# Kernel optimization log

Measured on AMD Instinct MI355X. Metric: run time of the kernel, lower is better.

The kernel has to match this reference:

```python
import jax, jax.numpy as jnp
import numpy as np

D, H, K = 384, 6, 8

def _ln(x, g, b, eps=1e-5):
    mu = jnp.mean(x, axis=-1, keepdims=True)
    var = jnp.mean((x - mu) ** 2, axis=-1, keepdims=True)
    return (x - mu) * jax.lax.rsqrt(var + eps) * g + b

def setup_inputs() -> dict:
    key = jax.random.key(0)
    ks = jax.random.split(key, 20)
    B, N = 4, 2048
    s = 0.02
    inp = {
        'x': jax.random.normal(ks[0], (B, N, D), jnp.float32),
        'knn_index': jax.random.randint(ks[1], (B * K * N,), 0, B * N, jnp.int64),
        'ln1_g': jnp.ones((D,), jnp.float32),
        'ln1_b': jnp.zeros((D,), jnp.float32),
        'w_qkv': jax.random.normal(ks[2], (D, 3 * D), jnp.float32) * s,
        'w_proj': jax.random.normal(ks[3], (D, D), jnp.float32) * s,
        'b_proj': jnp.zeros((D,), jnp.float32),
        'w_knn': jax.random.normal(ks[4], (2 * D, D), jnp.float32) * s,
        'b_knn': jnp.zeros((D,), jnp.float32),
        'w_g1': jax.random.normal(ks[5], (2 * D, D), jnp.float32) * s,
        'b_g1': jnp.zeros((D,), jnp.float32),
        'w_g2': jax.random.normal(ks[6], (D, D), jnp.float32) * s,
        'b_g2': jnp.zeros((D,), jnp.float32),
        'ln2_g': jnp.ones((D,), jnp.float32),
        'ln2_b': jnp.zeros((D,), jnp.float32),
        'w_fc1': jax.random.normal(ks[7], (D, 4 * D), jnp.float32) * s,
        'b_fc1': jnp.zeros((4 * D,), jnp.float32),
        'w_fc2': jax.random.normal(ks[8], (4 * D, D), jnp.float32) * s,
        'b_fc2': jnp.zeros((D,), jnp.float32),
    }
    return inp

def reference(x, knn_index, ln1_g, ln1_b, w_qkv, w_proj, b_proj, w_knn, b_knn,
              w_g1, b_g1, w_g2, b_g2, ln2_g, ln2_b, w_fc1, b_fc1, w_fc2, b_fc2):
    B, N, _ = x.shape
    hd = D // H
    scale = hd ** -0.5
    nx = _ln(x, ln1_g, ln1_b)
    # --- self attention ---
    qkv = (nx @ w_qkv).reshape(B, N, 3, H, hd).transpose(2, 0, 3, 1, 4)  # [3,B,H,N,hd]
    q, k, v = qkv[0], qkv[1], qkv[2]
    attn = jax.nn.softmax(jnp.einsum('bhnd,bhmd->bhnm', q * scale, k), axis=-1)
    attn_out = jnp.einsum('bhnm,bhmd->bhnd', attn, v).transpose(0, 2, 1, 3).reshape(B, N, D)
    attn_out = attn_out @ w_proj + b_proj
    # --- EdgeConv-style graph feature: gather-concat-MLP-maxpool ---
    feat = nx.reshape(B * N, D)[knn_index].reshape(B, K, N, D)
    xe = jnp.broadcast_to(nx[:, None], (B, K, N, D))
    gf = jnp.concatenate([feat - xe, xe], axis=-1)  # [B,K,N,2D]
    knn_out = jnp.max(jax.nn.leaky_relu(gf @ w_knn + b_knn, 0.2), axis=1)  # [B,N,D]
    # --- salience gate ---
    gi = jnp.concatenate([attn_out, knn_out], axis=-1)
    gate = jax.nn.sigmoid(jax.nn.gelu(gi @ w_g1 + b_g1, approximate=False) @ w_g2 + b_g2)
    fused = (1 - gate) * attn_out + gate * knn_out
    x = x + fused
    # --- FFN ---
    h = jax.nn.gelu(_ln(x, ln2_g, ln2_b) @ w_fc1 + b_fc1, approximate=False)
    x = x + (h @ w_fc2 + b_fc2)
    return x
```

## Files before the change

kernel.cpp:

```cpp
#include <hip/hip_runtime.h>
#include <math.h>

typedef unsigned short u16;
typedef __attribute__((ext_vector_type(8))) short short8;
typedef __attribute__((ext_vector_type(4))) float floatx4;
typedef __attribute__((ext_vector_type(4))) short sh4v;

union sh4u { sh4v v; u16 u[4]; };
union sh8u { short8 v; u16 u[8]; };

__device__ __forceinline__ floatx4 mfma16(short8 a, short8 b, floatx4 c) {
  return __builtin_amdgcn_mfma_f32_16x16x32_bf16(a, b, c, 0, 0, 0);
}

__device__ __forceinline__ floatx4 zero4() {
  floatx4 z = {0.f, 0.f, 0.f, 0.f};
  return z;
}

__device__ __forceinline__ u16 f2b(float f) {
  union { float f; unsigned u; } v; v.f = f;
  unsigned u = v.u;
  return (u16)((u + 0x7FFFu + ((u >> 16) & 1u)) >> 16);
}

__device__ __forceinline__ float b2f(u16 u) {
  union { unsigned u; float f; } v; v.u = ((unsigned)u) << 16;
  return v.f;
}

__device__ __forceinline__ float gelu_exact(float x) {
  return 0.5f * x * (1.f + erff(x * 0.70710678118654752440f));
}

__device__ __forceinline__ unsigned pack2(float a, float b) {
  return (unsigned)f2b(a) | ((unsigned)f2b(b) << 16);
}

__device__ __forceinline__ unsigned permpack(float p0, float p1) {
  return __builtin_amdgcn_perm(__float_as_uint(p1), __float_as_uint(p0), 0x07060302u);
}

__global__ __launch_bounds__(256) void tcln_kernel(
    const float* __restrict__ p0, const float* __restrict__ p1,
    const float* __restrict__ p2, const float* __restrict__ p3,
    const float* __restrict__ p4, const float* __restrict__ p5,
    const float* __restrict__ wknn,
    u16* __restrict__ o0, u16* __restrict__ o1, u16* __restrict__ o2,
    u16* __restrict__ o3, u16* __restrict__ o4, u16* __restrict__ o5,
    u16* __restrict__ wcT,
    const float* __restrict__ x, const float* __restrict__ g,
    const float* __restrict__ bia, u16* __restrict__ nx) {
  __shared__ u16 L[64][66];
  int t = blockIdx.x, tid = threadIdx.x;
  if (t >= 612) {
    int wave = tid >> 6, lane = tid & 63;
    int row = (t - 612) * 4 + wave;
    const float* xr = x + (size_t)row * 384;
    float v[6];
    float s = 0.f;
#pragma unroll
    for (int j = 0; j < 6; j++) { v[j] = xr[lane + 64 * j]; s += v[j]; }
#pragma unroll
    for (int off = 32; off > 0; off >>= 1) s += __shfl_xor(s, off);
    float mu = s * (1.f / 384.f);
    float ss = 0.f;
#pragma unroll
    for (int j = 0; j < 6; j++) { float d = v[j] - mu; ss += d * d; }
#pragma unroll
    for (int off = 32; off > 0; off >>= 1) ss += __shfl_xor(ss, off);
    float rstd = rsqrtf(ss * (1.f / 384.f) + 1e-5f);
    u16* orow = nx + (size_t)row * 384;
#pragma unroll
    for (int j = 0; j < 6; j++) {
      int d = lane + 64 * j;
      orow[d] = f2b((v[j] - mu) * rstd * g[d] + bia[d]);
    }
    return;
  }
  if (t >= 540) {
    t -= 540;
    int tk = t / 12, tn = t % 12;
    int k0 = tk * 64, j0 = tn * 64;
#pragma unroll
    for (int i = 0; i < 4; i++) {
      int c = tid + 256 * i;
      int r = c >> 4, c4 = (c & 15) * 4;
      floatx4 v;
      if (j0 < 384) {
        v = *(const floatx4*)(wknn + (size_t)(k0 + r) * 384 + j0 + c4);
      } else {
        floatx4 a = *(const floatx4*)(wknn + (size_t)(384 + k0 + r) * 384 + (j0 - 384) + c4);
        floatx4 b = *(const floatx4*)(wknn + (size_t)(k0 + r) * 384 + (j0 - 384) + c4);
        v = a - b;
      }
      *(unsigned*)&L[r][c4]     = pack2(v[0], v[1]);
      *(unsigned*)&L[r][c4 + 2] = pack2(v[2], v[3]);
    }
    __syncthreads();
#pragma unroll
    for (int i = 0; i < 2; i++) {
      int c = tid + 256 * i;
      int nn = c >> 3, k8 = (c & 7) * 8;
      sh8u pk;
#pragma unroll
      for (int j = 0; j < 8; j++) pk.u[j] = L[k8 + j][nn];
      *(short8*)(wcT + (size_t)(j0 + nn) * 384 + k0 + k8) = pk.v;
    }
    return;
  }
  const float* src; u16* dst; int Kd, Nd, tk, tn;
  if      (t < 108) { src = p0; dst = o0; Kd = 384;  Nd = 1152; tk = t / 18; tn = t % 18; }
  else if (t < 144) { src = p1; dst = o1; Kd = 384;  Nd = 384;  t -= 108; tk = t / 6;  tn = t % 6; }
  else if (t < 216) { src = p2; dst = o2; Kd = 768;  Nd = 384;  t -= 144; tk = t / 6;  tn = t % 6; }
  else if (t < 252) { src = p3; dst = o3; Kd = 384;  Nd = 384;  t -= 216; tk = t / 6;  tn = t % 6; }
  else if (t < 396) { src = p4; dst = o4; Kd = 384;  Nd = 1536; t -= 252; tk = t / 24; tn = t % 24; }
  else              { src = p5; dst = o5; Kd = 1536; Nd = 384;  t -= 396; tk = t / 6;  tn = t % 6; }
  int k0 = tk * 64, n0 = tn * 64;
#pragma unroll
  for (int i = 0; i < 4; i++) {
    int c = tid + 256 * i;
    int r = c >> 4, c4 = (c & 15) * 4;
    floatx4 v = *(const floatx4*)(src + (size_t)(k0 + r) * Nd + n0 + c4);
    *(unsigned*)&L[r][c4]     = pack2(v[0], v[1]);
    *(unsigned*)&L[r][c4 + 2] = pack2(v[2], v[3]);
  }
  __syncthreads();
#pragma unroll
  for (int i = 0; i < 2; i++) {
    int c = tid + 256 * i;
    int nn = c >> 3, k8 = (c & 7) * 8;
    sh8u pk;
#pragma unroll
    for (int j = 0; j < 8; j++) pk.u[j] = L[k8 + j][nn];
    *(short8*)(dst + (size_t)(n0 + nn) * Kd + k0 + k8) = pk.v;
  }
}

__global__ __launch_bounds__(256) void ln_kernel(const float* __restrict__ x,
                                                 const float* __restrict__ g,
                                                 const float* __restrict__ bia,
                                                 u16* __restrict__ out) {
  int wave = threadIdx.x >> 6, lane = threadIdx.x & 63;
  int row = blockIdx.x * 4 + wave;
  const float* xr = x + (size_t)row * 384;
  float v[6];
  float s = 0.f;
#pragma unroll
  for (int j = 0; j < 6; j++) { v[j] = xr[lane + 64 * j]; s += v[j]; }
#pragma unroll
  for (int off = 32; off > 0; off >>= 1) s += __shfl_xor(s, off);
  float mu = s * (1.f / 384.f);
  float ss = 0.f;
#pragma unroll
  for (int j = 0; j < 6; j++) { float d = v[j] - mu; ss += d * d; }
#pragma unroll
  for (int off = 32; off > 0; off >>= 1) ss += __shfl_xor(ss, off);
  float rstd = rsqrtf(ss * (1.f / 384.f) + 1e-5f);
  u16* orow = out + (size_t)row * 384;
#pragma unroll
  for (int j = 0; j < 6; j++) {
    int d = lane + 64 * j;
    orow[d] = f2b((v[j] - mu) * rstd * g[d] + bia[d]);
  }
}

template <int EPI>
__global__ __launch_bounds__(256) void gemm128_kernel(
    const u16* __restrict__ A0, const u16* __restrict__ A1, int Ksplit,
    const u16* __restrict__ BwT, const u16* __restrict__ BwT2, int N, int K,
    const float* __restrict__ bias,
    float* __restrict__ outF, u16* __restrict__ outB, u16* __restrict__ outB2,
    const u16* __restrict__ eA16, const u16* __restrict__ eK16,
    const float* __restrict__ eX, u16* __restrict__ outV) {
  __shared__ u16 As[128][72];
  __shared__ u16 Bs[128][72];
  int tid = threadIdx.x;
  int lane = tid & 63, wave = tid >> 6, quad = lane >> 4, l16 = lane & 15;
  int n0 = blockIdx.x * 128, m0 = blockIdx.y * 128;
  int wm = (wave >> 1) * 64, wn = (wave & 1) * 64;
  const u16* Bsrc = BwT;
  int nbase = n0;
  if (EPI == 8 && n0 >= 1152) { Bsrc = BwT2; nbase = n0 - 1152; }
  floatx4 acc[4][4];
#pragma unroll
  for (int i = 0; i < 4; i++)
#pragma unroll
    for (int j = 0; j < 4; j++) acc[i][j] = zero4();

  for (int k0 = 0; k0 < K; k0 += 64) {
    const u16* Ap;
    int kk, sA;
    if (k0 < Ksplit) { Ap = A0; kk = k0; sA = Ksplit; }
    else             { Ap = A1; kk = k0 - Ksplit; sA = K - Ksplit; }
#pragma unroll
    for (int i = 0; i < 4; i++) {
      int c = tid + 256 * i;
      int row = c >> 3, c8 = (c & 7) * 8;
      *(short8*)&As[row][c8] =
          *(const short8*)(Ap + (size_t)(m0 + row) * sA + kk + c8);
      *(short8*)&Bs[row][c8] =
          *(const short8*)(Bsrc + (size_t)(nbase + row) * K + k0 + c8);
    }
    __syncthreads();
#pragma unroll
    for (int kh = 0; kh < 2; kh++) {
      short8 af[4], bfr[4];
#pragma unroll
      for (int ti = 0; ti < 4; ti++)
        af[ti] = *(const short8*)&As[wm + ti * 16 + l16][kh * 32 + quad * 8];
#pragma unroll
      for (int tj = 0; tj < 4; tj++)
        bfr[tj] = *(const short8*)&Bs[wn + tj * 16 + l16][kh * 32 + quad * 8];
#pragma unroll
      for (int ti = 0; ti < 4; ti++)
#pragma unroll
        for (int tj = 0; tj < 4; tj++)
          acc[ti][tj] = mfma16(af[ti], bfr[tj], acc[ti][tj]);
    }
    __syncthreads();
  }

#pragma unroll
  for (int ti = 0; ti < 4; ti++)
#pragma unroll
    for (int tj = 0; tj < 4; tj++) {
      int col = n0 + wn + tj * 16 + l16;
      int row0 = m0 + wm + ti * 16 + quad * 4;
      if (EPI == 8) {
        if (n0 < 1152) {
          float sc = (col < 384) ? 0.18033688011112042f : 1.f;
          sh4u pk;
#pragma unroll
          for (int r = 0; r < 4; r++) {
            u16 bv = f2b(acc[ti][tj][r] * sc);
            outB[(size_t)(row0 + r) * 1152 + col] = bv;
            pk.u[r] = bv;
          }
          if (col >= 768) {
            int b = row0 >> 11, n = row0 & 2047;
            int hd = col - 768;
            *(sh4v*)(outV + ((size_t)(b * 6 + (hd >> 6)) * 64 + (hd & 63)) * 2048 + n) = pk.v;
          }
        } else {
#pragma unroll
          for (int r = 0; r < 4; r++)
            outB2[(size_t)(row0 + r) * 768 + (col - 1152)] = f2b(acc[ti][tj][r]);
        }
      } else {
#pragma unroll
        for (int r = 0; r < 4; r++) {
          size_t rc = (size_t)(row0 + r) * N + col;
          float v = acc[ti][tj][r];
          if (EPI == 3) {
            outB[rc] = f2b(gelu_exact(v + bias[col]));
          } else if (EPI == 4) {
            float gte = 1.f / (1.f + __expf(-(v + bias[col])));
            float fu = (1.f - gte) * b2f(eA16[rc]) + gte * b2f(eK16[rc]);
            outF[rc] = eX[rc] + fu;
          } else if (EPI == 5) {
            outF[rc] = v + bias[col] + eX[rc];
          }
        }
      }
    }
}

__global__ __launch_bounds__(256) void attn1_kernel(const u16* __restrict__ qkv,
                                                    const u16* __restrict__ Vt,
                                                    u16* __restrict__ OPb,
                                                    float* __restrict__ LS) {
  __shared__ u16 Ks[64][72];
  __shared__ u16 Vts[64][72];
  __shared__ u16 Ps[4][32][72];
  int tid = threadIdx.x;
  int lane = tid & 63, w = tid >> 6, quad = lane >> 4, l16 = lane & 15;
  int bh = blockIdx.y, b = bh / 6, h = bh % 6;
  int q0 = blockIdx.x * 128, split = blockIdx.z;
  const u16* qbase = qkv + (size_t)b * 2048 * 1152 + h * 64;
  const u16* kbase = qbase + 384 + (size_t)split * 1024 * 1152;
  const u16* vtb = Vt + (size_t)bh * 64 * 2048 + split * 1024;
  short8 qf[2][2];
#pragma unroll
  for (int s = 0; s < 2; s++) {
    int qrow = q0 + w * 32 + s * 16 + l16;
    qf[s][0] = *(const short8*)(qbase + (size_t)qrow * 1152 + quad * 8);
    qf[s][1] = *(const short8*)(qbase + (size_t)qrow * 1152 + 32 + quad * 8);
  }
  floatx4 O[4][2];
  float lsum[2] = {0.f, 0.f};
#pragma unroll
  for (int i = 0; i < 4; i++)
#pragma unroll
    for (int s = 0; s < 2; s++) O[i][s] = zero4();

  int rb = tid >> 3, c8 = (tid & 7) * 8;
  short8 rk[2], rv[2];
  rk[0] = *(const short8*)(kbase + (size_t)rb * 1152 + c8);
  rk[1] = *(const short8*)(kbase + (size_t)(rb + 32) * 1152 + c8);
  rv[0] = *(const short8*)(vtb + (size_t)rb * 2048 + c8);
  rv[1] = *(const short8*)(vtb + (size_t)(rb + 32) * 2048 + c8);

  for (int kt = 0; kt < 16; kt++) {
    __syncthreads();
    *(short8*)&Ks[rb][c8] = rk[0];
    *(short8*)&Ks[rb + 32][c8] = rk[1];
    *(short8*)&Vts[rb][c8] = rv[0];
    *(short8*)&Vts[rb + 32][c8] = rv[1];
    __syncthreads();
    if (kt < 15) {
      int key0 = (kt + 1) * 64;
      rk[0] = *(const short8*)(kbase + (size_t)(key0 + rb) * 1152 + c8);
      rk[1] = *(const short8*)(kbase + (size_t)(key0 + rb + 32) * 1152 + c8);
      rv[0] = *(const short8*)(vtb + (size_t)rb * 2048 + key0 + c8);
      rv[1] = *(const short8*)(vtb + (size_t)(rb + 32) * 2048 + key0 + c8);
    }
#pragma unroll
    for (int mt = 0; mt < 4; mt++) {
      short8 k0 = *(const short8*)&Ks[mt * 16 + l16][quad * 8];
      short8 k1 = *(const short8*)&Ks[mt * 16 + l16][32 + quad * 8];
#pragma unroll
      for (int s = 0; s < 2; s++) {
        floatx4 st = mfma16(k0, qf[s][0], zero4());
        st = mfma16(k1, qf[s][1], st);
        float p0 = exp2f(st[0]), p1 = exp2f(st[1]);
        float p2 = exp2f(st[2]), p3 = exp2f(st[3]);
        lsum[s] += (p0 + p1) + (p2 + p3);
        uint2 pk;
        pk.x = permpack(p0, p1);
        pk.y = permpack(p2, p3);
        *(uint2*)&Ps[w][s * 16 + l16][mt * 16 + quad * 4] = pk;
      }
    }
    short8 pf[2][2];
#pragma unroll
    for (int s = 0; s < 2; s++) {
      pf[s][0] = *(const short8*)&Ps[w][s * 16 + l16][quad * 8];
      pf[s][1] = *(const short8*)&Ps[w][s * 16 + l16][32 + quad * 8];
    }
#pragma unroll
    for (int mt2 = 0; mt2 < 4; mt2++) {
      short8 v0 = *(const short8*)&Vts[mt2 * 16 + l16][quad * 8];
      short8 v1 = *(const short8*)&Vts[mt2 * 16 + l16][32 + quad * 8];
#pragma unroll
      for (int s = 0; s < 2; s++) {
        O[mt2][s] = mfma16(v0, pf[s][0], O[mt2][s]);
        O[mt2][s] = mfma16(v1, pf[s][1], O[mt2][s]);
      }
    }
  }
#pragma unroll
  for (int s = 0; s < 2; s++) {
    lsum[s] += __shfl_xor(lsum[s], 16);
    lsum[s] += __shfl_xor(lsum[s], 32);
    int row = b * 2048 + q0 + w * 32 + s * 16 + l16;
    u16* orow = OPb + (size_t)split * 8192 * 384 + (size_t)row * 384 + h * 64;
#pragma unroll
    for (int mt2 = 0; mt2 < 4; mt2++) {
      sh4u pk;
#pragma unroll
      for (int r = 0; r < 4; r++) pk.u[r] = f2b(O[mt2][s][r]);
      *(sh4v*)(orow + mt2 * 16 + quad * 4) = pk.v;
    }
    if (quad == 0) LS[split * 8192 + row] = lsum[s];
  }
}

__global__ __launch_bounds__(256) void projknn_kernel(
    const u16* __restrict__ OPb, const float* __restrict__ LS,
    const u16* __restrict__ BwT, const float* __restrict__ bias,
    u16* __restrict__ outB,
    const u16* __restrict__ GBb, const int* __restrict__ kidx,
    const float* __restrict__ bknn, u16* __restrict__ knn_bf) {
  __shared__ u16 As[128][72];
  __shared__ u16 Bs[128][72];
  int bid = blockIdx.x, tid = threadIdx.x;
  if (bid >= 192) {
    int wave = tid >> 6, lane = tid & 63;
    int row = (bid - 192) * 4 + wave;
    int b = row >> 11, n = row & 2047;
    float base[6], acc[6];
#pragma unroll
    for (int j = 0; j < 6; j++) {
      int d = lane + 64 * j;
      base[j] = b2f(GBb[(size_t)row * 768 + 384 + d]) + bknn[d];
      acc[j] = -1e30f;
    }
    for (int kk = 0; kk < 8; kk++) {
      int g = kidx[(b * 8 + kk) * 2048 + n];
      const u16* Gr = GBb + (size_t)g * 768;
#pragma unroll
      for (int j = 0; j < 6; j++) {
        float v = b2f(Gr[lane + 64 * j]) + base[j];
        v = v > 0.f ? v : 0.2f * v;
        acc[j] = fmaxf(acc[j], v);
      }
    }
#pragma unroll
    for (int j = 0; j < 6; j++)
      knn_bf[(size_t)row * 384 + lane + 64 * j] = f2b(acc[j]);
    return;
  }
  int lane = tid & 63, wave = tid >> 6, quad = lane >> 4, l16 = lane & 15;
  int n0 = (bid % 3) * 128, m0 = (bid / 3) * 128;
  int wm = (wave >> 1) * 64, wn = (wave & 1) * 64;
  floatx4 acc[4][4];
#pragma unroll
  for (int i = 0; i < 4; i++)
#pragma unroll
    for (int j = 0; j < 4; j++) acc[i][j] = zero4();

  for (int k0 = 0; k0 < 384; k0 += 64) {
#pragma unroll
    for (int i = 0; i < 4; i++) {
      int c = tid + 256 * i;
      int row = c >> 3, c8 = (c & 7) * 8;
      int gr = m0 + row;
      float rl = 1.f / (LS[gr] + LS[8192 + gr]);
      const u16* p0 = OPb + (size_t)gr * 384 + k0 + c8;
      sh8u a0, a1, pk;
      a0.v = *(const short8*)p0;
      a1.v = *(const short8*)(p0 + (size_t)8192 * 384);
#pragma unroll
      for (int j = 0; j < 8; j++) pk.u[j] = f2b((b2f(a0.u[j]) + b2f(a1.u[j])) * rl);
      *(short8*)&As[row][c8] = pk.v;
      *(short8*)&Bs[row][c8] =
          *(const short8*)(BwT + (size_t)(n0 + row) * 384 + k0 + c8);
    }
    __syncthreads();
#pragma unroll
    for (int kh = 0; kh < 2; kh++) {
      short8 af[4], bfr[4];
#pragma unroll
      for (int ti = 0; ti < 4; ti++)
        af[ti] = *(const short8*)&As[wm + ti * 16 + l16][kh * 32 + quad * 8];
#pragma unroll
      for (int tj = 0; tj < 4; tj++)
        bfr[tj] = *(const short8*)&Bs[wn + tj * 16 + l16][kh * 32 + quad * 8];
#pragma unroll
      for (int ti = 0; ti < 4; ti++)
#pragma unroll
        for (int tj = 0; tj < 4; tj++)
          acc[ti][tj] = mfma16(af[ti], bfr[tj], acc[ti][tj]);
    }
    __syncthreads();
  }
#pragma unroll
  for (int ti = 0; ti < 4; ti++)
#pragma unroll
    for (int tj = 0; tj < 4; tj++) {
      int col = n0 + wn + tj * 16 + l16;
      int row0 = m0 + wm + ti * 16 + quad * 4;
#pragma unroll
      for (int r = 0; r < 4; r++)
        outB[(size_t)(row0 + r) * 384 + col] = f2b(acc[ti][tj][r] + bias[col]);
    }
}

extern "C" void kernel_launch(void* const* d_in, const int* in_sizes, int n_in,
                              void* d_out, int out_size, void* d_ws, size_t ws_size,
                              hipStream_t stream) {
  const float* x    = (const float*)d_in[0];
  const int* kidx   = (const int*)d_in[1];
  const float* ln1g = (const float*)d_in[2];
  const float* ln1b = (const float*)d_in[3];
  const float* wqkv = (const float*)d_in[4];
  const float* wproj= (const float*)d_in[5];
  const float* bproj= (const float*)d_in[6];
  const float* wknn = (const float*)d_in[7];
  const float* bknn = (const float*)d_in[8];
  const float* wg1  = (const float*)d_in[9];
  const float* bg1  = (const float*)d_in[10];
  const float* wg2  = (const float*)d_in[11];
  const float* bg2  = (const float*)d_in[12];
  const float* ln2g = (const float*)d_in[13];
  const float* ln2b = (const float*)d_in[14];
  const float* wfc1 = (const float*)d_in[15];
  const float* bfc1 = (const float*)d_in[16];
  const float* wfc2 = (const float*)d_in[17];
  const float* bfc2 = (const float*)d_in[18];
  float* out = (float*)d_out;

  const int M = 8192;
  char* ws = (char*)d_ws;
  size_t off = 0;
  auto alloc = [&](size_t bytes) -> char* {
    char* p = ws + off;
    off += (bytes + 255) & ~(size_t)255;
    return p;
  };
  u16* nx_bf    = (u16*)alloc((size_t)M * 384 * 2);
  u16* qkv_bf   = (u16*)alloc((size_t)M * 1152 * 2);
  u16* attn_bf  = (u16*)alloc((size_t)M * 384 * 2);
  u16* GBb      = (u16*)alloc((size_t)M * 768 * 2);
  u16* knn_bf   = (u16*)alloc((size_t)M * 384 * 2);
  float* x2     = (float*)alloc((size_t)M * 384 * 4);
  u16* t1_bf    = (u16*)alloc((size_t)M * 384 * 2);
  u16* nx2_bf   = (u16*)alloc((size_t)M * 384 * 2);
  u16* Vt_b     = (u16*)alloc((size_t)24 * 64 * 2048 * 2);
  u16* OPb      = (u16*)alloc((size_t)2 * M * 384 * 2);
  float* LS     = (float*)alloc((size_t)2 * M * 4);
  u16* wqkvT    = (u16*)alloc((size_t)1152 * 384 * 2);
  u16* wprojT   = (u16*)alloc(384 * 384 * 2);
  u16* wcT      = (u16*)alloc((size_t)768 * 384 * 2);
  u16* wg1T     = (u16*)alloc((size_t)384 * 768 * 2);
  u16* wg2T     = (u16*)alloc(384 * 384 * 2);
  u16* wfc1T    = (u16*)alloc((size_t)1536 * 384 * 2);
  u16* wfc2T    = (u16*)alloc((size_t)384 * 1536 * 2);
  u16* h_bf     = qkv_bf;

  tcln_kernel<<<2660, 256, 0, stream>>>(wqkv, wproj, wg1, wg2, wfc1, wfc2, wknn,
                                        wqkvT, wprojT, wg1T, wg2T, wfc1T, wfc2T, wcT,
                                        x, ln1g, ln1b, nx_bf);
  gemm128_kernel<8><<<dim3(15, 64), 256, 0, stream>>>(nx_bf, nx_bf, 384, wqkvT, wcT, 1920, 384,
                                                      nullptr, nullptr, qkv_bf, GBb,
                                                      nullptr, nullptr, nullptr, Vt_b);
  attn1_kernel<<<dim3(16, 24, 2), 256, 0, stream>>>(qkv_bf, Vt_b, OPb, LS);
  projknn_kernel<<<2240, 256, 0, stream>>>(OPb, LS, wprojT, bproj, attn_bf,
                                           GBb, kidx, bknn, knn_bf);
  gemm128_kernel<3><<<dim3(3, 64), 256, 0, stream>>>(attn_bf, knn_bf, 384, wg1T, nullptr, 384, 768,
                                                     bg1, nullptr, t1_bf, nullptr,
                                                     nullptr, nullptr, nullptr, nullptr);
  gemm128_kernel<4><<<dim3(3, 64), 256, 0, stream>>>(t1_bf, t1_bf, 384, wg2T, nullptr, 384, 384,
                                                     bg2, x2, nullptr, nullptr,
                                                     attn_bf, knn_bf, x, nullptr);
  ln_kernel<<<2048, 256, 0, stream>>>(x2, ln2g, ln2b, nx2_bf);
  gemm128_kernel<3><<<dim3(12, 64), 256, 0, stream>>>(nx2_bf, nx2_bf, 384, wfc1T, nullptr, 1536, 384,
                                                      bfc1, nullptr, h_bf, nullptr,
                                                      nullptr, nullptr, nullptr, nullptr);
  gemm128_kernel<5><<<dim3(3, 64), 256, 0, stream>>>(h_bf, h_bf, 1536, wfc2T, nullptr, 384, 1536,
                                                     bfc2, out, nullptr, nullptr,
                                                     nullptr, nullptr, x2, nullptr);
  (void)in_sizes; (void)n_in; (void)out_size; (void)ws_size;
}
```

Before: 314.4 us.

## Split attention keys four ways and store residual stream in bf16

The attention kernel now splits the key range into four chunks of 512 instead of two of 1024. This doubles the number of blocks and shortens each block's loop. The projection stage sums four partial outputs and four row sums to match. Separately, the intermediate residual x2 is stored as bf16 instead of fp32, which halves its memory traffic in the LN2 and FC2 epilogues. The cost is extra partial-sum traffic and lower precision in the residual path.

```diff
diff --git a/kernel.cpp b/kernel.cpp
--- a/kernel.cpp
+++ b/kernel.cpp
@@ -137,17 +137,17 @@
   }
 }
 
-__global__ __launch_bounds__(256) void ln_kernel(const float* __restrict__ x,
-                                                 const float* __restrict__ g,
-                                                 const float* __restrict__ bia,
-                                                 u16* __restrict__ out) {
+__global__ __launch_bounds__(256) void lnb_kernel(const u16* __restrict__ x,
+                                                  const float* __restrict__ g,
+                                                  const float* __restrict__ bia,
+                                                  u16* __restrict__ out) {
   int wave = threadIdx.x >> 6, lane = threadIdx.x & 63;
   int row = blockIdx.x * 4 + wave;
-  const float* xr = x + (size_t)row * 384;
+  const u16* xr = x + (size_t)row * 384;
   float v[6];
   float s = 0.f;
 #pragma unroll
-  for (int j = 0; j < 6; j++) { v[j] = xr[lane + 64 * j]; s += v[j]; }
+  for (int j = 0; j < 6; j++) { v[j] = b2f(xr[lane + 64 * j]); s += v[j]; }
 #pragma unroll
   for (int off = 32; off > 0; off >>= 1) s += __shfl_xor(s, off);
   float mu = s * (1.f / 384.f);
@@ -257,9 +257,9 @@
           } else if (EPI == 4) {
             float gte = 1.f / (1.f + __expf(-(v + bias[col])));
             float fu = (1.f - gte) * b2f(eA16[rc]) + gte * b2f(eK16[rc]);
-            outF[rc] = eX[rc] + fu;
-          } else if (EPI == 5) {
-            outF[rc] = v + bias[col] + eX[rc];
+            outB[rc] = f2b(eX[rc] + fu);
+          } else if (EPI == 7) {
+            outF[rc] = v + bias[col] + b2f(eA16[rc]);
           }
         }
       }
@@ -278,8 +278,8 @@
   int bh = blockIdx.y, b = bh / 6, h = bh % 6;
   int q0 = blockIdx.x * 128, split = blockIdx.z;
   const u16* qbase = qkv + (size_t)b * 2048 * 1152 + h * 64;
-  const u16* kbase = qbase + 384 + (size_t)split * 1024 * 1152;
-  const u16* vtb = Vt + (size_t)bh * 64 * 2048 + split * 1024;
+  const u16* kbase = qbase + 384 + (size_t)split * 512 * 1152;
+  const u16* vtb = Vt + (size_t)bh * 64 * 2048 + split * 512;
   short8 qf[2][2];
 #pragma unroll
   for (int s = 0; s < 2; s++) {
@@ -301,14 +301,14 @@
   rv[0] = *(const short8*)(vtb + (size_t)rb * 2048 + c8);
   rv[1] = *(const short8*)(vtb + (size_t)(rb + 32) * 2048 + c8);
 
-  for (int kt = 0; kt < 16; kt++) {
+  for (int kt = 0; kt < 8; kt++) {
     __syncthreads();
     *(short8*)&Ks[rb][c8] = rk[0];
     *(short8*)&Ks[rb + 32][c8] = rk[1];
     *(short8*)&Vts[rb][c8] = rv[0];
     *(short8*)&Vts[rb + 32][c8] = rv[1];
     __syncthreads();
-    if (kt < 15) {
+    if (kt < 7) {
       int key0 = (kt + 1) * 64;
       rk[0] = *(const short8*)(kbase + (size_t)(key0 + rb) * 1152 + c8);
       rk[1] = *(const short8*)(kbase + (size_t)(key0 + rb + 32) * 1152 + c8);
@@ -410,19 +410,23 @@
 #pragma unroll
     for (int j = 0; j < 4; j++) acc[i][j] = zero4();
 
+  const size_t SP = (size_t)8192 * 384;
   for (int k0 = 0; k0 < 384; k0 += 64) {
 #pragma unroll
     for (int i = 0; i < 4; i++) {
       int c = tid + 256 * i;
       int row = c >> 3, c8 = (c & 7) * 8;
       int gr = m0 + row;
-      float rl = 1.f / (LS[gr] + LS[8192 + gr]);
+      float rl = 1.f / ((LS[gr] + LS[8192 + gr]) + (LS[16384 + gr] + LS[24576 + gr]));
       const u16* p0 = OPb + (size_t)gr * 384 + k0 + c8;
-      sh8u a0, a1, pk;
+      sh8u a0, a1, a2, a3, pk;
       a0.v = *(const short8*)p0;
-      a1.v = *(const short8*)(p0 + (size_t)8192 * 384);
-#pragma unroll
-      for (int j = 0; j < 8; j++) pk.u[j] = f2b((b2f(a0.u[j]) + b2f(a1.u[j])) * rl);
+      a1.v = *(const short8*)(p0 + SP);
+      a2.v = *(const short8*)(p0 + 2 * SP);
+      a3.v = *(const short8*)(p0 + 3 * SP);
+#pragma unroll
+      for (int j = 0; j < 8; j++)
+        pk.u[j] = f2b(((b2f(a0.u[j]) + b2f(a1.u[j])) + (b2f(a2.u[j]) + b2f(a3.u[j]))) * rl);
       *(short8*)&As[row][c8] = pk.v;
       *(short8*)&Bs[row][c8] =
           *(const short8*)(BwT + (size_t)(n0 + row) * 384 + k0 + c8);
@@ -494,12 +498,12 @@
   u16* attn_bf  = (u16*)alloc((size_t)M * 384 * 2);
   u16* GBb      = (u16*)alloc((size_t)M * 768 * 2);
   u16* knn_bf   = (u16*)alloc((size_t)M * 384 * 2);
-  float* x2     = (float*)alloc((size_t)M * 384 * 4);
+  u16* x2b      = (u16*)alloc((size_t)M * 384 * 2);
   u16* t1_bf    = (u16*)alloc((size_t)M * 384 * 2);
   u16* nx2_bf   = (u16*)alloc((size_t)M * 384 * 2);
   u16* Vt_b     = (u16*)alloc((size_t)24 * 64 * 2048 * 2);
-  u16* OPb      = (u16*)alloc((size_t)2 * M * 384 * 2);
-  float* LS     = (float*)alloc((size_t)2 * M * 4);
+  u16* OPb      = (u16*)alloc((size_t)4 * M * 384 * 2);
+  float* LS     = (float*)alloc((size_t)4 * M * 4);
   u16* wqkvT    = (u16*)alloc((size_t)1152 * 384 * 2);
   u16* wprojT   = (u16*)alloc(384 * 384 * 2);
   u16* wcT      = (u16*)alloc((size_t)768 * 384 * 2);
@@ -515,21 +519,21 @@
   gemm128_kernel<8><<<dim3(15, 64), 256, 0, stream>>>(nx_bf, nx_bf, 384, wqkvT, wcT, 1920, 384,
                                                       nullptr, nullptr, qkv_bf, GBb,
                                                       nullptr, nullptr, nullptr, Vt_b);
-  attn1_kernel<<<dim3(16, 24, 2), 256, 0, stream>>>(qkv_bf, Vt_b, OPb, LS);
+  attn1_kernel<<<dim3(16, 24, 4), 256, 0, stream>>>(qkv_bf, Vt_b, OPb, LS);
   projknn_kernel<<<2240, 256, 0, stream>>>(OPb, LS, wprojT, bproj, attn_bf,
                                            GBb, kidx, bknn, knn_bf);
   gemm128_kernel<3><<<dim3(3, 64), 256, 0, stream>>>(attn_bf, knn_bf, 384, wg1T, nullptr, 384, 768,
                                                      bg1, nullptr, t1_bf, nullptr,
                                                      nullptr, nullptr, nullptr, nullptr);
   gemm128_kernel<4><<<dim3(3, 64), 256, 0, stream>>>(t1_bf, t1_bf, 384, wg2T, nullptr, 384, 384,
-                                                     bg2, x2, nullptr, nullptr,
+                                                     bg2, nullptr, x2b, nullptr,
                                                      attn_bf, knn_bf, x, nullptr);
-  ln_kernel<<<2048, 256, 0, stream>>>(x2, ln2g, ln2b, nx2_bf);
+  lnb_kernel<<<2048, 256, 0, stream>>>(x2b, ln2g, ln2b, nx2_bf);
   gemm128_kernel<3><<<dim3(12, 64), 256, 0, stream>>>(nx2_bf, nx2_bf, 384, wfc1T, nullptr, 1536, 384,
                                                       bfc1, nullptr, h_bf, nullptr,
                                                       nullptr, nullptr, nullptr, nullptr);
-  gemm128_kernel<5><<<dim3(3, 64), 256, 0, stream>>>(h_bf, h_bf, 1536, wfc2T, nullptr, 384, 1536,
+  gemm128_kernel<7><<<dim3(3, 64), 256, 0, stream>>>(h_bf, h_bf, 1536, wfc2T, nullptr, 384, 1536,
                                                      bfc2, out, nullptr, nullptr,
-                                                     nullptr, nullptr, x2, nullptr);
+                                                     x2b, nullptr, nullptr, nullptr);
   (void)in_sizes; (void)n_in; (void)out_size; (void)ws_size;
 }
```

Result: no change. 313.7 us (-0.2%).
